# Performance work log

Hardware: AMD Instinct MI355X
Metric: run time of the kernel (lower is better)

## Reference

```python
import jax, jax.numpy as jnp
import numpy as np

N_E = 16384
E_DIM = 256
SRC_DIM = 1024
BETA = 0.25


def setup_inputs() -> dict:
    key = jax.random.key(0)
    k_x, k_ew, k_eb, k_cb, k_dw, k_db = jax.random.split(key, 6)
    x = jax.random.normal(k_x, (16, 576, SRC_DIM), dtype=jnp.float32)
    # encoder Linear(source_dim -> embed_dim)
    enc_w = jax.random.normal(k_ew, (SRC_DIM, E_DIM), dtype=jnp.float32) / np.sqrt(SRC_DIM)
    enc_b = jax.random.normal(k_eb, (E_DIM,), dtype=jnp.float32) * 0.01
    # codebook initialized uniform(-1/n_e, 1/n_e) as in the torch module
    codebook = jax.random.uniform(k_cb, (N_E, E_DIM), dtype=jnp.float32, minval=-1.0 / N_E, maxval=1.0 / N_E)
    # decoder Linear(embed_dim -> source_dim)
    dec_w = jax.random.normal(k_dw, (E_DIM, SRC_DIM), dtype=jnp.float32) / np.sqrt(E_DIM)
    dec_b = jax.random.normal(k_db, (SRC_DIM,), dtype=jnp.float32) * 0.01
    return {"x": x, "enc_w": enc_w, "enc_b": enc_b, "codebook": codebook, "dec_w": dec_w, "dec_b": dec_b}


def reference(x, enc_w, enc_b, codebook, dec_w, dec_b):
    # encode: [B,S,src] -> [B,S,e]
    z = jnp.einsum('bsd,de->bse', x, enc_w) + enc_b
    # squared distances to all codebook entries: ||z||^2 + ||E||^2 - 2 z.E^T
    z2 = jnp.sum(z * z, axis=-1, keepdims=True)            # [B,S,1]
    e2 = jnp.sum(codebook * codebook, axis=-1)             # [n_e]
    cross = jnp.einsum('bse,ne->bsn', z, codebook)         # [B,S,n_e]
    d = z2 + e2 - 2.0 * cross
    idx = jnp.argmin(d, axis=-1)                           # [B,S] int
    z_q = codebook[idx]                                    # [B,S,e]
    sg = jax.lax.stop_gradient
    loss = BETA * jnp.mean((sg(z_q) - z) ** 2) + jnp.mean((z_q - sg(z)) ** 2)
    z_q_st = z + sg(z_q - z)                               # straight-through
    out = jnp.einsum('bse,ed->bsd', z_q_st, dec_w) + dec_b
    return (out, loss)
```

## Files before the change

kernel.cpp:

```cpp
#include <hip/hip_runtime.h>

typedef __bf16 bf16;
typedef __bf16 bf16x8 __attribute__((ext_vector_type(8)));
typedef float f32x4 __attribute__((ext_vector_type(4)));
typedef unsigned int u32;
typedef long long i64;
typedef i64 i64x2 __attribute__((ext_vector_type(2)));
typedef unsigned char u8;

#define N_TOK 9216
#define SRC 1024
#define EDIM 256
#define NE 16384
#define GROUPS 16
#define GSIZE 1024
#define NBLK_GATHER 2304
#define CB_SCALE 8192.0f
#define NEG_TWO_OVER_SCALE -2.44140625e-4f
#define LOSS_DENOM 2359296.0f

__device__ __forceinline__ void async_load16(const void* g, void* l) {
  __builtin_amdgcn_global_load_lds(
      (__attribute__((address_space(1))) void*)(void*)(const_cast<void*>(g)),
      (__attribute__((address_space(3))) void*)l, 16, 0, 0);
}

__device__ __forceinline__ f32x4 mfma16(bf16x8 a, bf16x8 b, f32x4 c) {
  return __builtin_amdgcn_mfma_f32_16x16x32_bf16(a, b, c, 0, 0, 0);
}
__device__ __forceinline__ f32x4 mfma_fp8(i64 a, i64 b, f32x4 c) {
  return __builtin_amdgcn_mfma_f32_16x16x32_fp8_fp8(a, b, c, 0, 0, 0);
}

__global__ __launch_bounds__(256) void k_prep(const float* __restrict__ enc_w,
                                              const float* __restrict__ dec_w,
                                              const float* __restrict__ cb,
                                              bf16* __restrict__ enc_wT,
                                              bf16* __restrict__ dec_wT,
                                              u32* __restrict__ cbb8,
                                              float* __restrict__ e2p) {
  int b = blockIdx.x;
  if (b < 1024) {
    int id = b * 256 + threadIdx.x;
    {
      int n = id >> 10, k = id & 1023;
      enc_wT[id] = (bf16)enc_w[k * EDIM + n];
    }
    {
      int n = id >> 8, k = id & 255;
      dec_wT[id] = (bf16)dec_w[k * SRC + n];
    }
  } else {
    int row = (b - 1024) * 4 + (threadIdx.x >> 6);
    int lane = threadIdx.x & 63;
    int slot = lane >> 2;
    int h = slot ^ (row & 15);
    int bo = (lane & 3) * 4;
    int s = 2 * (h & 3) + (bo >> 3);
    int k0 = s * 32 + (h >> 2) * 8 + (bo & 7);
    float4 v = *(const float4*)(cb + (size_t)row * EDIM + k0);
    int pk = __builtin_amdgcn_cvt_pk_fp8_f32(v.x * CB_SCALE, v.y * CB_SCALE, 0, false);
    pk = __builtin_amdgcn_cvt_pk_fp8_f32(v.z * CB_SCALE, v.w * CB_SCALE, pk, true);
    cbb8[(size_t)row * 64 + lane] = (u32)pk;
    float sq = v.x * v.x + v.y * v.y + v.z * v.z + v.w * v.w;
#pragma unroll
    for (int off = 32; off; off >>= 1) sq += __shfl_xor(sq, off, 64);
    if (lane == 0) e2p[row] = sq + 1.0f;
  }
}

template <int BN, bool AF32>
__global__ __launch_bounds__(256) void k_gemm(const void* __restrict__ Ap,
                                              const bf16* __restrict__ BT,
                                              const float* __restrict__ bias,
                                              float* __restrict__ Cf,
                                              u8* __restrict__ C8, int K, int N) {
  __shared__ __align__(16) bf16 As[2][128 * 32];
  __shared__ __align__(16) bf16 Bs[2][BN * 32];
  const int tid = threadIdx.x;
  const int wid = tid >> 6, lane = tid & 63;
  const int col = lane & 15, quad = lane >> 4;
  constexpr int WN = BN / 2, UN = BN / 32;
  const int wm = (wid >> 1) * 64, wn = (wid & 1) * WN;
  const int bm = blockIdx.x * 128, bn = blockIdx.y * BN;
  const bf16* Ab = (const bf16*)Ap;
  const float* Af = (const float*)Ap;
  f32x4 acc[4][UN] = {};

  const int ar0 = tid >> 2, ag0 = tid & 3;
  const int ar1 = ar0 + 64;

  auto stageB = [&](int kc, int bb) {
#pragma unroll
    for (int j = 0; j < BN / 64; j++) {
      int slot = wid * (BN / 64) * 64 + j * 64 + lane;
      int row = slot >> 2;
      int gg = (slot & 3) ^ (row & 3);
      async_load16(BT + (size_t)(bn + row) * K + kc + gg * 8,
                   (char*)&Bs[bb][0] + wid * (BN / 64) * 1024 + j * 1024);
    }
  };
  auto stageA_async = [&](int kc, int bb) {
#pragma unroll
    for (int j = 0; j < 2; j++) {
      int slot = wid * 128 + j * 64 + lane;
      int row = slot >> 2;
      int gg = (slot & 3) ^ (row & 3);
      async_load16(Ab + (size_t)(bm + row) * K + kc + gg * 8,
                   (char*)&As[bb][0] + wid * 2048 + j * 1024);
    }
  };

  float4 p0, p1, p2, p3;
  auto loadA_f32 = [&](int kc) {
    const float* a0 = Af + (size_t)(bm + ar0) * K + kc + ag0 * 8;
    const float* a1 = Af + (size_t)(bm + ar1) * K + kc + ag0 * 8;
    p0 = *(const float4*)a0;
    p1 = *(const float4*)(a0 + 4);
    p2 = *(const float4*)a1;
    p3 = *(const float4*)(a1 + 4);
  };
  auto writeA_f32 = [&](int bb) {
    bf16x8 o0 = {(bf16)p0.x, (bf16)p0.y, (bf16)p0.z, (bf16)p0.w,
                 (bf16)p1.x, (bf16)p1.y, (bf16)p1.z, (bf16)p1.w};
    bf16x8 o1 = {(bf16)p2.x, (bf16)p2.y, (bf16)p2.z, (bf16)p2.w,
                 (bf16)p3.x, (bf16)p3.y, (bf16)p3.z, (bf16)p3.w};
    *(bf16x8*)((char*)&As[bb][0] + (ar0 * 4 + (ag0 ^ (ar0 & 3))) * 16) = o0;
    *(bf16x8*)((char*)&As[bb][0] + (ar1 * 4 + (ag0 ^ (ar1 & 3))) * 16) = o1;
  };

  const int iters = K / 32;
  if (AF32) {
    loadA_f32(0);
    writeA_f32(0);
  } else {
    stageA_async(0, 0);
  }
  stageB(0, 0);

  for (int it = 0; it < iters; it++) {
    int cbuf = it & 1, nbuf = cbuf ^ 1;
    if (AF32 && it + 1 < iters) loadA_f32((it + 1) * 32);
    __syncthreads();
    if (it + 1 < iters) {
      if (!AF32) stageA_async((it + 1) * 32, nbuf);
      stageB((it + 1) * 32, nbuf);
    }
    bf16x8 afr[4], bfr[UN];
#pragma unroll
    for (int t = 0; t < 4; t++) {
      int row = wm + t * 16 + col;
      afr[t] = *(const bf16x8*)((const char*)&As[cbuf][0] +
                                (row * 4 + (quad ^ (row & 3))) * 16);
    }
#pragma unroll
    for (int u = 0; u < UN; u++) {
      int row = wn + u * 16 + col;
      bfr[u] = *(const bf16x8*)((const char*)&Bs[cbuf][0] +
                                (row * 4 + (quad ^ (row & 3))) * 16);
    }
#pragma unroll
    for (int t = 0; t < 4; t++)
#pragma unroll
      for (int u = 0; u < UN; u++) acc[t][u] = mfma16(afr[t], bfr[u], acc[t][u]);
    if (AF32 && it + 1 < iters) writeA_f32(nbuf);
  }

#pragma unroll
  for (int u = 0; u < UN; u++) {
    int n = bn + wn + u * 16 + col;
    float bv = bias[n];
#pragma unroll
    for (int t = 0; t < 4; t++) {
#pragma unroll
      for (int r = 0; r < 4; r++) {
        int m = bm + wm + t * 16 + quad * 4 + r;
        float v = acc[t][u][r] + bv;
        if (Cf) Cf[(size_t)m * N + n] = v;
        if (C8) {
          int pk = __builtin_amdgcn_cvt_pk_fp8_f32(v, v, 0, false);
          C8[(size_t)m * N + n] = (u8)(pk & 0xFF);
        }
      }
    }
  }
}

__global__ __launch_bounds__(256, 3) void k_argmin(const u8* __restrict__ zb8,
                                                   const u8* __restrict__ cbb8,
                                                   const float* __restrict__ e2p,
                                                   float* __restrict__ pval,
                                                   int* __restrict__ pidx) {
  __shared__ __align__(16) u8 Cs[2 * 16384];
  const int tid = threadIdx.x;
  const int wid = tid >> 6, lane = tid & 63;
  const int col = lane & 15, quad = lane >> 4;
  const int g = blockIdx.y;
  const int tw = blockIdx.x * 192 + wid * 48;

  i64 af[3][8];
#pragma unroll
  for (int t = 0; t < 3; t++)
#pragma unroll
    for (int s = 0; s < 8; s++)
      af[t][s] = *(const i64*)(zb8 + (size_t)(tw + t * 16 + col) * EDIM + s * 32 + quad * 8);

  u32 best[3][4];
#pragma unroll
  for (int t = 0; t < 3; t++)
#pragma unroll
    for (int r = 0; r < 4; r++) best[t][r] = 0xFFFFFFFFu;

  auto stage_load = [&](int st, int bb) {
    const u8* src = cbb8 + (size_t)(g * GSIZE + st * 64) * EDIM;
#pragma unroll
    for (int j = 0; j < 4; j++) {
      async_load16(src + (wid * 256 + j * 64 + lane) * 16,
                   (char*)Cs + bb * 16384 + wid * 4096 + j * 1024);
    }
  };

  auto compute = [&](int st, int bb) {
    const char* bbase = (const char*)Cs + bb * 16384;
    const int cb0 = g * GSIZE + st * 64;
    float ev[4];
#pragma unroll
    for (int u = 0; u < 4; u++) ev[u] = e2p[cb0 + u * 16 + col];
    f32x4 c[3][4] = {};
#pragma unroll
    for (int s2 = 0; s2 < 4; s2++) {
#pragma unroll
      for (int u = 0; u < 4; u++) {
        int row = u * 16 + col;
        i64x2 bb2 = *(const i64x2*)(bbase + row * 256 + (((quad * 4 + s2) ^ col) * 16));
#pragma unroll
        for (int t = 0; t < 3; t++) {
          c[t][u] = mfma_fp8(af[t][2 * s2], bb2.x, c[t][u]);
          c[t][u] = mfma_fp8(af[t][2 * s2 + 1], bb2.y, c[t][u]);
        }
      }
    }
#pragma unroll
    for (int u = 0; u < 4; u++) {
      u32 iv = (u32)(st * 4 + u);
#pragma unroll
      for (int t = 0; t < 3; t++)
#pragma unroll
        for (int r = 0; r < 4; r++) {
          u32 du = __float_as_uint(fmaf(c[t][u][r], NEG_TWO_OVER_SCALE, ev[u]));
          u32 key = (du & 0xFFFFFFC0u) | iv;
          best[t][r] = key < best[t][r] ? key : best[t][r];
        }
    }
  };

  stage_load(0, 0);
  for (int st = 0; st < 16; st++) {
    __syncthreads();
    if (st < 15) stage_load(st + 1, (st + 1) & 1);
    compute(st, st & 1);
  }

#pragma unroll
  for (int t = 0; t < 3; t++)
#pragma unroll
    for (int r = 0; r < 4; r++) {
      u32 key = best[t][r];
      int cw = col;
#pragma unroll
      for (int off = 1; off < 16; off <<= 1) {
        u32 ok = (u32)__shfl_xor((int)key, off, 64);
        int oc = __shfl_xor(cw, off, 64);
        if (ok < key) { key = ok; cw = oc; }
      }
      if (col == 0) {
        int token = tw + t * 16 + quad * 4 + r;
        pval[token * GROUPS + g] = __uint_as_float(key & 0xFFFFFFC0u);
        pidx[token * GROUPS + g] = g * GSIZE + (int)(key & 63u) * 16 + cw;
      }
    }
}

__global__ __launch_bounds__(256) void k_gather(const float* __restrict__ cb,
                                                const u8* __restrict__ zb8,
                                                const float* __restrict__ pval,
                                                const int* __restrict__ pidx,
                                                bf16* __restrict__ zqb,
                                                float* __restrict__ lpart) {
  __shared__ float ls[4];
  int wv = threadIdx.x >> 6;
  int token = blockIdx.x * 4 + wv;
  int lane = threadIdx.x & 63;
  float v = 3.4e38f;
  int idx = 0;
  if (lane < 16) {
    v = pval[token * GROUPS + lane];
    idx = pidx[token * GROUPS + lane];
  }
#pragma unroll
  for (int off = 1; off < 16; off <<= 1) {
    float ov = __shfl_xor(v, off, 64);
    int oi = __shfl_xor(idx, off, 64);
    if (ov < v || (ov == v && oi < idx)) { v = ov; idx = oi; }
  }
  idx = __shfl(idx, 0, 64);
  float4 q = ((const float4*)(cb + (size_t)idx * EDIM))[lane];
  u32 zw = *(const u32*)(zb8 + (size_t)token * EDIM + lane * 4);
  float z0 = __builtin_amdgcn_cvt_f32_fp8(zw, 0);
  float z1 = __builtin_amdgcn_cvt_f32_fp8(zw, 1);
  float z2 = __builtin_amdgcn_cvt_f32_fp8(zw, 2);
  float z3 = __builtin_amdgcn_cvt_f32_fp8(zw, 3);
  bf16* zq = zqb + (size_t)token * EDIM + lane * 4;
  zq[0] = (bf16)q.x;
  zq[1] = (bf16)q.y;
  zq[2] = (bf16)q.z;
  zq[3] = (bf16)q.w;
  float dx = q.x - z0, dy = q.y - z1, dz = q.z - z2, dw = q.w - z3;
  float s = dx * dx + dy * dy + dz * dz + dw * dw;
#pragma unroll
  for (int off = 32; off; off >>= 1) s += __shfl_xor(s, off, 64);
  if (lane == 0) ls[wv] = s;
  __syncthreads();
  if (threadIdx.x == 0) lpart[blockIdx.x] = ls[0] + ls[1] + ls[2] + ls[3];
}

__global__ __launch_bounds__(256) void k_loss(const float* __restrict__ lpart,
                                              float* __restrict__ outl) {
  __shared__ float ls[4];
  float s = 0.f;
  for (int i = threadIdx.x; i < NBLK_GATHER; i += 256) s += lpart[i];
#pragma unroll
  for (int off = 32; off; off >>= 1) s += __shfl_xor(s, off, 64);
  int wv = threadIdx.x >> 6;
  if ((threadIdx.x & 63) == 0) ls[wv] = s;
  __syncthreads();
  if (threadIdx.x == 0) *outl = 1.25f * (ls[0] + ls[1] + ls[2] + ls[3]) / LOSS_DENOM;
}

extern "C" void kernel_launch(void* const* d_in, const int* in_sizes, int n_in,
                              void* d_out, int out_size, void* d_ws, size_t ws_size,
                              hipStream_t stream) {
  const float* x = (const float*)d_in[0];
  const float* enc_w = (const float*)d_in[1];
  const float* enc_b = (const float*)d_in[2];
  const float* cb = (const float*)d_in[3];
  const float* dec_w = (const float*)d_in[4];
  const float* dec_b = (const float*)d_in[5];
  float* out = (float*)d_out;
  float* out_loss = out + (size_t)N_TOK * SRC;

  char* ws = (char*)d_ws;
  bf16* enc_wT = (bf16*)(ws + 0);
  bf16* dec_wT = (bf16*)(ws + 524288);
  u8* zb8 = (u8*)(ws + 1048576);
  u32* cbb8 = (u32*)(ws + 3407872);
  float* e2p = (float*)(ws + 7602176);
  float* pval = (float*)(ws + 7667712);
  int* pidx = (int*)(ws + 8257536);
  bf16* zqb = (bf16*)(ws + 8847360);
  float* lpart = (float*)(ws + 13565952);

  k_prep<<<5120, 256, 0, stream>>>(enc_w, dec_w, cb, enc_wT, dec_wT, cbb8, e2p);
  k_gemm<64, true><<<dim3(72, 4), 256, 0, stream>>>(x, enc_wT, enc_b, nullptr, zb8,
                                                    1024, 256);
  k_argmin<<<dim3(48, GROUPS), 256, 0, stream>>>(zb8, (const u8*)cbb8, e2p, pval, pidx);
  k_gather<<<NBLK_GATHER, 256, 0, stream>>>(cb, zb8, pval, pidx, zqb, lpart);
  k_gemm<128, false><<<dim3(72, 8), 256, 0, stream>>>(zqb, dec_wT, dec_b, out, nullptr,
                                                      256, 1024);
  k_loss<<<1, 256, 0, stream>>>(lpart, out_loss);
}
```

Before: 216.5 us.

## Use 16x16x128 scaled FP8 MFMA for argmin and retile encoder/decoder GEMMs

The argmin distance kernel moves from the 16x16x32 FP8 MFMA to the gfx950 16x16x128 scaled f8f6f4 MFMA. The -2/scale factor is folded into the codebook quantisation and the e2 term is pre-scaled, so the epilogue becomes a single add instead of an fma. The codebook swizzle layout changes to match the wider K fragments. The generic templated GEMM is split into dedicated encoder (64x128 tile) and decoder (64x256 tile) kernels with more blocks, to improve occupancy and wave count. This trades fewer MFMA issues for changed LDS access patterns and higher register use per fragment.

```diff
diff --git a/kernel.cpp b/kernel.cpp
--- a/kernel.cpp
+++ b/kernel.cpp
@@ -3,9 +3,8 @@
 typedef __bf16 bf16;
 typedef __bf16 bf16x8 __attribute__((ext_vector_type(8)));
 typedef float f32x4 __attribute__((ext_vector_type(4)));
+typedef int i32x8 __attribute__((ext_vector_type(8)));
 typedef unsigned int u32;
-typedef long long i64;
-typedef i64 i64x2 __attribute__((ext_vector_type(2)));
 typedef unsigned char u8;
 
 #define N_TOK 9216
@@ -15,8 +14,8 @@
 #define GROUPS 16
 #define GSIZE 1024
 #define NBLK_GATHER 2304
-#define CB_SCALE 8192.0f
-#define NEG_TWO_OVER_SCALE -2.44140625e-4f
+#define NEG_CB_SCALE -8192.0f
+#define E2_SCALE 4096.0f
 #define LOSS_DENOM 2359296.0f
 
 __device__ __forceinline__ void async_load16(const void* g, void* l) {
@@ -28,8 +27,9 @@
 __device__ __forceinline__ f32x4 mfma16(bf16x8 a, bf16x8 b, f32x4 c) {
   return __builtin_amdgcn_mfma_f32_16x16x32_bf16(a, b, c, 0, 0, 0);
 }
-__device__ __forceinline__ f32x4 mfma_fp8(i64 a, i64 b, f32x4 c) {
-  return __builtin_amdgcn_mfma_f32_16x16x32_fp8_fp8(a, b, c, 0, 0, 0);
+__device__ __forceinline__ f32x4 mfma_mx(i32x8 a, i32x8 b, f32x4 c) {
+  return __builtin_amdgcn_mfma_scale_f32_16x16x128_f8f6f4(
+      a, b, c, 0, 0, 0, 0x7F7F7F7F, 0, 0x7F7F7F7F);
 }
 
 __global__ __launch_bounds__(256) void k_prep(const float* __restrict__ enc_w,
@@ -38,7 +38,7 @@
                                               bf16* __restrict__ enc_wT,
                                               bf16* __restrict__ dec_wT,
                                               u32* __restrict__ cbb8,
-                                              float* __restrict__ e2p) {
+                                              float* __restrict__ e2s) {
   int b = blockIdx.x;
   if (b < 1024) {
     int id = b * 256 + threadIdx.x;
@@ -54,141 +54,101 @@
     int row = (b - 1024) * 4 + (threadIdx.x >> 6);
     int lane = threadIdx.x & 63;
     int slot = lane >> 2;
-    int h = slot ^ (row & 15);
-    int bo = (lane & 3) * 4;
-    int s = 2 * (h & 3) + (bo >> 3);
-    int k0 = s * 32 + (h >> 2) * 8 + (bo & 7);
+    int h = (slot & 8) | ((slot & 7) ^ (row & 7));
+    int k0 = h * 16 + (lane & 3) * 4;
     float4 v = *(const float4*)(cb + (size_t)row * EDIM + k0);
-    int pk = __builtin_amdgcn_cvt_pk_fp8_f32(v.x * CB_SCALE, v.y * CB_SCALE, 0, false);
-    pk = __builtin_amdgcn_cvt_pk_fp8_f32(v.z * CB_SCALE, v.w * CB_SCALE, pk, true);
+    int pk = __builtin_amdgcn_cvt_pk_fp8_f32(v.x * NEG_CB_SCALE, v.y * NEG_CB_SCALE, 0, false);
+    pk = __builtin_amdgcn_cvt_pk_fp8_f32(v.z * NEG_CB_SCALE, v.w * NEG_CB_SCALE, pk, true);
     cbb8[(size_t)row * 64 + lane] = (u32)pk;
     float sq = v.x * v.x + v.y * v.y + v.z * v.z + v.w * v.w;
 #pragma unroll
     for (int off = 32; off; off >>= 1) sq += __shfl_xor(sq, off, 64);
-    if (lane == 0) e2p[row] = sq + 1.0f;
-  }
-}
-
-template <int BN, bool AF32>
-__global__ __launch_bounds__(256) void k_gemm(const void* __restrict__ Ap,
-                                              const bf16* __restrict__ BT,
-                                              const float* __restrict__ bias,
-                                              float* __restrict__ Cf,
-                                              u8* __restrict__ C8, int K, int N) {
-  __shared__ __align__(16) bf16 As[2][128 * 32];
-  __shared__ __align__(16) bf16 Bs[2][BN * 32];
+    if (lane == 0) e2s[row] = E2_SCALE * (sq + 1.0f);
+  }
+}
+
+__global__ __launch_bounds__(256) void k_enc(const float* __restrict__ x,
+                                             const bf16* __restrict__ wT,
+                                             const float* __restrict__ bias,
+                                             u8* __restrict__ z8) {
+  __shared__ __align__(16) bf16 As[2][64 * 32];
+  __shared__ __align__(16) bf16 Bs[2][128 * 32];
   const int tid = threadIdx.x;
   const int wid = tid >> 6, lane = tid & 63;
   const int col = lane & 15, quad = lane >> 4;
-  constexpr int WN = BN / 2, UN = BN / 32;
-  const int wm = (wid >> 1) * 64, wn = (wid & 1) * WN;
-  const int bm = blockIdx.x * 128, bn = blockIdx.y * BN;
-  const bf16* Ab = (const bf16*)Ap;
-  const float* Af = (const float*)Ap;
-  f32x4 acc[4][UN] = {};
-
-  const int ar0 = tid >> 2, ag0 = tid & 3;
-  const int ar1 = ar0 + 64;
-
+  const int wm = (wid >> 1) * 32, wn = (wid & 1) * 64;
+  const int bm = blockIdx.x * 64, bn = blockIdx.y * 128;
+  f32x4 acc[2][4] = {};
+  const int arow = tid >> 2, ags = tid & 3;
+
+  float4 q0, q1;
+  auto loadA = [&](int kc) {
+    const float* p = x + (size_t)(bm + arow) * SRC + kc + ags * 8;
+    q0 = *(const float4*)p;
+    q1 = *(const float4*)(p + 4);
+  };
+  auto writeA = [&](int bb) {
+    bf16x8 o = {(bf16)q0.x, (bf16)q0.y, (bf16)q0.z, (bf16)q0.w,
+                (bf16)q1.x, (bf16)q1.y, (bf16)q1.z, (bf16)q1.w};
+    *(bf16x8*)((char*)&As[bb][0] + (arow * 4 + (ags ^ (arow & 3))) * 16) = o;
+  };
   auto stageB = [&](int kc, int bb) {
-#pragma unroll
-    for (int j = 0; j < BN / 64; j++) {
-      int slot = wid * (BN / 64) * 64 + j * 64 + lane;
-      int row = slot >> 2;
-      int gg = (slot & 3) ^ (row & 3);
-      async_load16(BT + (size_t)(bn + row) * K + kc + gg * 8,
-                   (char*)&Bs[bb][0] + wid * (BN / 64) * 1024 + j * 1024);
-    }
-  };
-  auto stageA_async = [&](int kc, int bb) {
 #pragma unroll
     for (int j = 0; j < 2; j++) {
       int slot = wid * 128 + j * 64 + lane;
       int row = slot >> 2;
       int gg = (slot & 3) ^ (row & 3);
-      async_load16(Ab + (size_t)(bm + row) * K + kc + gg * 8,
-                   (char*)&As[bb][0] + wid * 2048 + j * 1024);
-    }
-  };
-
-  float4 p0, p1, p2, p3;
-  auto loadA_f32 = [&](int kc) {
-    const float* a0 = Af + (size_t)(bm + ar0) * K + kc + ag0 * 8;
-    const float* a1 = Af + (size_t)(bm + ar1) * K + kc + ag0 * 8;
-    p0 = *(const float4*)a0;
-    p1 = *(const float4*)(a0 + 4);
-    p2 = *(const float4*)a1;
-    p3 = *(const float4*)(a1 + 4);
-  };
-  auto writeA_f32 = [&](int bb) {
-    bf16x8 o0 = {(bf16)p0.x, (bf16)p0.y, (bf16)p0.z, (bf16)p0.w,
-                 (bf16)p1.x, (bf16)p1.y, (bf16)p1.z, (bf16)p1.w};
-    bf16x8 o1 = {(bf16)p2.x, (bf16)p2.y, (bf16)p2.z, (bf16)p2.w,
-                 (bf16)p3.x, (bf16)p3.y, (bf16)p3.z, (bf16)p3.w};
-    *(bf16x8*)((char*)&As[bb][0] + (ar0 * 4 + (ag0 ^ (ar0 & 3))) * 16) = o0;
-    *(bf16x8*)((char*)&As[bb][0] + (ar1 * 4 + (ag0 ^ (ar1 & 3))) * 16) = o1;
-  };
-
-  const int iters = K / 32;
-  if (AF32) {
-    loadA_f32(0);
-    writeA_f32(0);
-  } else {
-    stageA_async(0, 0);
-  }
+      async_load16(wT + (size_t)(bn + row) * SRC + kc + gg * 8,
+                   (char*)&Bs[bb][0] + wid * 2048 + j * 1024);
+    }
+  };
+
+  loadA(0);
+  writeA(0);
   stageB(0, 0);
-
-  for (int it = 0; it < iters; it++) {
+  for (int it = 0; it < 32; it++) {
     int cbuf = it & 1, nbuf = cbuf ^ 1;
-    if (AF32 && it + 1 < iters) loadA_f32((it + 1) * 32);
+    if (it < 31) loadA((it + 1) * 32);
     __syncthreads();
-    if (it + 1 < iters) {
-      if (!AF32) stageA_async((it + 1) * 32, nbuf);
-      stageB((it + 1) * 32, nbuf);
-    }
-    bf16x8 afr[4], bfr[UN];
-#pragma unroll
-    for (int t = 0; t < 4; t++) {
+    if (it < 31) stageB((it + 1) * 32, nbuf);
+    bf16x8 afr[2], bfr[4];
+#pragma unroll
+    for (int t = 0; t < 2; t++) {
       int row = wm + t * 16 + col;
       afr[t] = *(const bf16x8*)((const char*)&As[cbuf][0] +
                                 (row * 4 + (quad ^ (row & 3))) * 16);
     }
 #pragma unroll
-    for (int u = 0; u < UN; u++) {
+    for (int u = 0; u < 4; u++) {
       int row = wn + u * 16 + col;
       bfr[u] = *(const bf16x8*)((const char*)&Bs[cbuf][0] +
                                 (row * 4 + (quad ^ (row & 3))) * 16);
     }
 #pragma unroll
-    for (int t = 0; t < 4; t++)
-#pragma unroll
-      for (int u = 0; u < UN; u++) acc[t][u] = mfma16(afr[t], bfr[u], acc[t][u]);
-    if (AF32 && it + 1 < iters) writeA_f32(nbuf);
-  }
-
-#pragma unroll
-  for (int u = 0; u < UN; u++) {
+    for (int t = 0; t < 2; t++)
+#pragma unroll
+      for (int u = 0; u < 4; u++) acc[t][u] = mfma16(afr[t], bfr[u], acc[t][u]);
+    if (it < 31) writeA(nbuf);
+  }
+#pragma unroll
+  for (int u = 0; u < 4; u++) {
     int n = bn + wn + u * 16 + col;
     float bv = bias[n];
 #pragma unroll
-    for (int t = 0; t < 4; t++) {
+    for (int t = 0; t < 2; t++)
 #pragma unroll
       for (int r = 0; r < 4; r++) {
         int m = bm + wm + t * 16 + quad * 4 + r;
         float v = acc[t][u][r] + bv;
-        if (Cf) Cf[(size_t)m * N + n] = v;
-        if (C8) {
-          int pk = __builtin_amdgcn_cvt_pk_fp8_f32(v, v, 0, false);
-          C8[(size_t)m * N + n] = (u8)(pk & 0xFF);
-        }
+        int pk = __builtin_amdgcn_cvt_pk_fp8_f32(v, v, 0, false);
+        z8[(size_t)m * EDIM + n] = (u8)(pk & 0xFF);
       }
-    }
   }
 }
 
 __global__ __launch_bounds__(256, 3) void k_argmin(const u8* __restrict__ zb8,
                                                    const u8* __restrict__ cbb8,
-                                                   const float* __restrict__ e2p,
+                                                   const float* __restrict__ e2s,
                                                    float* __restrict__ pval,
                                                    int* __restrict__ pidx) {
   __shared__ __align__(16) u8 Cs[2 * 16384];
@@ -198,12 +158,16 @@
   const int g = blockIdx.y;
   const int tw = blockIdx.x * 192 + wid * 48;
 
-  i64 af[3][8];
+  i32x8 af[3][2];
 #pragma unroll
   for (int t = 0; t < 3; t++)
 #pragma unroll
-    for (int s = 0; s < 8; s++)
-      af[t][s] = *(const i64*)(zb8 + (size_t)(tw + t * 16 + col) * EDIM + s * 32 + quad * 8);
+    for (int m = 0; m < 2; m++) {
+      const u8* p = zb8 + (size_t)(tw + t * 16 + col) * EDIM + m * 128 + quad * 32;
+      int4 lo = *(const int4*)p;
+      int4 hi = *(const int4*)(p + 16);
+      af[t][m] = (i32x8){lo.x, lo.y, lo.z, lo.w, hi.x, hi.y, hi.z, hi.w};
+    }
 
   u32 best[3][4];
 #pragma unroll
@@ -225,19 +189,21 @@
     const int cb0 = g * GSIZE + st * 64;
     float ev[4];
 #pragma unroll
-    for (int u = 0; u < 4; u++) ev[u] = e2p[cb0 + u * 16 + col];
+    for (int u = 0; u < 4; u++) ev[u] = e2s[cb0 + u * 16 + col];
     f32x4 c[3][4] = {};
-#pragma unroll
-    for (int s2 = 0; s2 < 4; s2++) {
+    const int r7 = col & 7;
+#pragma unroll
+    for (int m = 0; m < 2; m++) {
 #pragma unroll
       for (int u = 0; u < 4; u++) {
         int row = u * 16 + col;
-        i64x2 bb2 = *(const i64x2*)(bbase + row * 256 + (((quad * 4 + s2) ^ col) * 16));
-#pragma unroll
-        for (int t = 0; t < 3; t++) {
-          c[t][u] = mfma_fp8(af[t][2 * s2], bb2.x, c[t][u]);
-          c[t][u] = mfma_fp8(af[t][2 * s2 + 1], bb2.y, c[t][u]);
-        }
+        int s0 = m * 8 + ((2 * quad) ^ r7);
+        int s1 = m * 8 + ((2 * quad + 1) ^ r7);
+        int4 b0 = *(const int4*)(bbase + row * 256 + s0 * 16);
+        int4 b1 = *(const int4*)(bbase + row * 256 + s1 * 16);
+        i32x8 bfr = (i32x8){b0.x, b0.y, b0.z, b0.w, b1.x, b1.y, b1.z, b1.w};
+#pragma unroll
+        for (int t = 0; t < 3; t++) c[t][u] = mfma_mx(af[t][m], bfr, c[t][u]);
       }
     }
 #pragma unroll
@@ -247,7 +213,7 @@
       for (int t = 0; t < 3; t++)
 #pragma unroll
         for (int r = 0; r < 4; r++) {
-          u32 du = __float_as_uint(fmaf(c[t][u][r], NEG_TWO_OVER_SCALE, ev[u]));
+          u32 du = __float_as_uint(c[t][u][r] + ev[u]);
           u32 key = (du & 0xFFFFFFC0u) | iv;
           best[t][r] = key < best[t][r] ? key : best[t][r];
         }
@@ -324,6 +290,78 @@
   if (threadIdx.x == 0) lpart[blockIdx.x] = ls[0] + ls[1] + ls[2] + ls[3];
 }
 
+__global__ __launch_bounds__(256) void k_dec(const bf16* __restrict__ A,
+                                             const bf16* __restrict__ wT,
+                                             const float* __restrict__ bias,
+                                             float* __restrict__ out) {
+  __shared__ __align__(16) bf16 As[2][64 * 32];
+  __shared__ __align__(16) bf16 Bs[2][256 * 32];
+  const int tid = threadIdx.x;
+  const int wid = tid >> 6, lane = tid & 63;
+  const int col = lane & 15, quad = lane >> 4;
+  const int wm = (wid >> 1) * 32, wn = (wid & 1) * 128;
+  const int bm = blockIdx.x * 64, bn = blockIdx.y * 256;
+  f32x4 acc[2][8] = {};
+
+  auto stageA = [&](int kc, int bb) {
+    int slot = wid * 64 + lane;
+    int row = slot >> 2;
+    int gg = (slot & 3) ^ (row & 3);
+    async_load16(A + (size_t)(bm + row) * EDIM + kc + gg * 8,
+                 (char*)&As[bb][0] + wid * 1024);
+  };
+  auto stageB = [&](int kc, int bb) {
+#pragma unroll
+    for (int j = 0; j < 4; j++) {
+      int slot = wid * 256 + j * 64 + lane;
+      int row = slot >> 2;
+      int gg = (slot & 3) ^ (row & 3);
+      async_load16(wT + (size_t)(bn + row) * EDIM + kc + gg * 8,
+                   (char*)&Bs[bb][0] + wid * 4096 + j * 1024);
+    }
+  };
+
+  stageA(0, 0);
+  stageB(0, 0);
+  for (int it = 0; it < 8; it++) {
+    int cbuf = it & 1, nbuf = cbuf ^ 1;
+    __syncthreads();
+    if (it < 7) {
+      stageA((it + 1) * 32, nbuf);
+      stageB((it + 1) * 32, nbuf);
+    }
+    bf16x8 afr[2], bfr[8];
+#pragma unroll
+    for (int t = 0; t < 2; t++) {
+      int row = wm + t * 16 + col;
+      afr[t] = *(const bf16x8*)((const char*)&As[cbuf][0] +
+                                (row * 4 + (quad ^ (row & 3))) * 16);
+    }
+#pragma unroll
+    for (int u = 0; u < 8; u++) {
+      int row = wn + u * 16 + col;
+      bfr[u] = *(const bf16x8*)((const char*)&Bs[cbuf][0] +
+                                (row * 4 + (quad ^ (row & 3))) * 16);
+    }
+#pragma unroll
+    for (int t = 0; t < 2; t++)
+#pragma unroll
+      for (int u = 0; u < 8; u++) acc[t][u] = mfma16(afr[t], bfr[u], acc[t][u]);
+  }
+#pragma unroll
+  for (int u = 0; u < 8; u++) {
+    int n = bn + wn + u * 16 + col;
+    float bv = bias[n];
+#pragma unroll
+    for (int t = 0; t < 2; t++)
+#pragma unroll
+      for (int r = 0; r < 4; r++) {
+        int m = bm + wm + t * 16 + quad * 4 + r;
+        out[(size_t)m * SRC + n] = acc[t][u][r] + bv;
+      }
+  }
+}
+
 __global__ __launch_bounds__(256) void k_loss(const float* __restrict__ lpart,
                                               float* __restrict__ outl) {
   __shared__ float ls[4];
@@ -354,18 +392,16 @@
   bf16* dec_wT = (bf16*)(ws + 524288);
   u8* zb8 = (u8*)(ws + 1048576);
   u32* cbb8 = (u32*)(ws + 3407872);
-  float* e2p = (float*)(ws + 7602176);
+  float* e2s = (float*)(ws + 7602176);
   float* pval = (float*)(ws + 7667712);
   int* pidx = (int*)(ws + 8257536);
   bf16* zqb = (bf16*)(ws + 8847360);
   float* lpart = (float*)(ws + 13565952);
 
-  k_prep<<<5120, 256, 0, stream>>>(enc_w, dec_w, cb, enc_wT, dec_wT, cbb8, e2p);
-  k_gemm<64, true><<<dim3(72, 4), 256, 0, stream>>>(x, enc_wT, enc_b, nullptr, zb8,
-                                                    1024, 256);
-  k_argmin<<<dim3(48, GROUPS), 256, 0, stream>>>(zb8, (const u8*)cbb8, e2p, pval, pidx);
+  k_prep<<<5120, 256, 0, stream>>>(enc_w, dec_w, cb, enc_wT, dec_wT, cbb8, e2s);
+  k_enc<<<dim3(144, 2), 256, 0, stream>>>(x, enc_wT, enc_b, zb8);
+  k_argmin<<<dim3(48, GROUPS), 256, 0, stream>>>(zb8, (const u8*)cbb8, e2s, pval, pidx);
   k_gather<<<NBLK_GATHER, 256, 0, stream>>>(cb, zb8, pval, pidx, zqb, lpart);
-  k_gemm<128, false><<<dim3(72, 8), 256, 0, stream>>>(zqb, dec_wT, dec_b, out, nullptr,
-                                                      256, 1024);
+  k_dec<<<dim3(144, 4), 256, 0, stream>>>(zqb, dec_wT, dec_b, out);
   k_loss<<<1, 256, 0, stream>>>(lpart, out_loss);
 }
```

Measured after the change: 199.9 us. -7.7%, faster.
